# Performance work log

Hardware: AMD Instinct MI355X
Metric: run time of the kernel (lower is better)

Reference implementation:

```python
import jax, jax.numpy as jnp
import numpy as np

MARGIN = 0.25
SCALE = 64.0
OP = 1.0 + MARGIN
ON = -MARGIN
DELTA_P = 1.0 - MARGIN
DELTA_N = MARGIN
NEG_FILL = -1e4  # effectively -inf for these logits (|logit| < ~300)

B, D = 8192, 1024
N_IDS = 512


def setup_inputs() -> dict:
    key = jax.random.key(0)
    k1, k2 = jax.random.split(key)
    inputs = jax.random.normal(k1, (B, D), dtype=jnp.float32)
    targets = jax.random.randint(k2, (B,), 0, N_IDS, dtype=jnp.int64)
    return {"inputs": inputs, "targets": targets}


def reference(inputs, targets):
    # L2-normalize embeddings (torch F.normalize uses eps=1e-12 clamp on norm)
    norm = jnp.maximum(jnp.linalg.norm(inputs, axis=1, keepdims=True), 1e-12)
    x = inputs / norm
    sim = x @ x.T  # [B, B] cosine similarities

    same = targets[:, None] == targets[None, :]
    eye = jnp.eye(targets.shape[0], dtype=bool)
    pos_mask = same & ~eye
    neg_mask = ~same

    sim_sg = jax.lax.stop_gradient(sim)  # .detach() in original
    ap = jnp.maximum(OP - sim_sg, 0.0)
    an = jnp.maximum(sim_sg - ON, 0.0)

    logit_p = -ap * (sim - DELTA_P) * SCALE
    logit_n = an * (sim - DELTA_N) * SCALE

    lse_p = jax.nn.logsumexp(jnp.where(pos_mask, logit_p, NEG_FILL), axis=1)
    lse_n = jax.nn.logsumexp(jnp.where(neg_mask, logit_n, NEG_FILL), axis=1)

    loss_i = jax.nn.softplus(lse_n + lse_p)  # [B]
    valid = pos_mask.any(axis=1) & neg_mask.any(axis=1)

    total = jnp.sum(jnp.where(valid, loss_i, 0.0))
    count = jnp.maximum(jnp.sum(valid), 1)
    return total / count
```

## Files before the change

kernel.cpp:

```cpp
#include <hip/hip_runtime.h>
#include <hip/hip_bf16.h>
#include <math.h>

#define THREADS 256
typedef unsigned short ushortT;
typedef __attribute__((ext_vector_type(8))) short bf16x8;
typedef __attribute__((ext_vector_type(4))) float f32x4;

__device__ __forceinline__ void async16(const ushortT* g, ushortT* l) {
  __builtin_amdgcn_global_load_lds(
      (const __attribute__((address_space(1))) unsigned int*)g,
      (__attribute__((address_space(3))) unsigned int*)l, 16, 0, 0);
}

__device__ __forceinline__ ushortT f2bf(float f) {
  __hip_bfloat16 h = __float2bfloat16(f);
  return *reinterpret_cast<ushortT*>(&h);
}

__global__ __launch_bounds__(THREADS) void k_prep(const float* __restrict__ x,
                                                  ushortT* __restrict__ xn, int D) {
  __shared__ float red[4];
  const int row = blockIdx.x;
  const int tid = threadIdx.x;
  const int gid = row * (D / 4) + tid;
  const float4 v = reinterpret_cast<const float4*>(x)[gid];
  float s = v.x * v.x + v.y * v.y + v.z * v.z + v.w * v.w;
  #pragma unroll
  for (int off = 32; off; off >>= 1) s += __shfl_xor(s, off);
  if ((tid & 63) == 0) red[tid >> 6] = s;
  __syncthreads();
  const float tot = red[0] + red[1] + red[2] + red[3];
  const float rn = 1.0f / fmaxf(sqrtf(tot), 1e-12f);
  ushort4 o;
  o.x = f2bf(v.x * rn); o.y = f2bf(v.y * rn);
  o.z = f2bf(v.z * rn); o.w = f2bf(v.w * rn);
  reinterpret_cast<ushort4*>(xn)[gid] = o;
}

__global__ __launch_bounds__(THREADS, 3) void k_main_mfma(const ushortT* __restrict__ xn,
                                                          const int* __restrict__ tgt,
                                                          float4* __restrict__ partial,
                                                          int D, int nb) {
  __shared__ ushortT Asm[128 * 32];
  __shared__ ushortT Bsm[128 * 32];

  const int tid = threadIdx.x;
  const int lane = tid & 63;
  const int w = tid >> 6;

  const int b = blockIdx.x;
  int bi = (int)((2.f * nb + 1.f -
                  sqrtf((2.f * nb + 1.f) * (2.f * nb + 1.f) - 8.f * (float)b)) * 0.5f);
  while ((bi + 1) * (2 * nb - bi) / 2 <= b) ++bi;
  while (bi * (2 * nb - bi + 1) / 2 > b) --bi;
  const int bj = bi + (b - bi * (2 * nb - bi + 1) / 2);
  const bool isdiag = (bi == bj);

  const int i0 = bi * 128, j0 = bj * 128;
  const int wr = (w >> 1) * 64, wc = (w & 1) * 64;

  const int sr = lane & 15, sc = lane >> 4;
  const ushortT* gA0 = xn + (size_t)(i0 + w * 16 + sr) * D + sc * 8;
  const ushortT* gA1 = gA0 + (size_t)64 * D;
  const ushortT* gB0 = xn + (size_t)(j0 + w * 16 + sr) * D + sc * 8;
  const ushortT* gB1 = gB0 + (size_t)64 * D;
  ushortT* lA0 = &Asm[w * 512];
  ushortT* lA1 = &Asm[(w + 4) * 512];
  ushortT* lB0 = &Bsm[w * 512];
  ushortT* lB1 = &Bsm[(w + 4) * 512];

  const ushortT* Bbase = isdiag ? Asm : Bsm;
  const int aoff = ((w >> 1) * 4) * 512 + lane * 8;
  const int boff = ((w & 1) * 4) * 512 + lane * 8;

  f32x4 acc[4][4];
  #pragma unroll
  for (int mt = 0; mt < 4; ++mt)
    #pragma unroll
    for (int nt = 0; nt < 4; ++nt)
      acc[mt][nt] = (f32x4){0.f, 0.f, 0.f, 0.f};

  const int kiters = D / 32;
  for (int kk = 0; kk < kiters; ++kk) {
    const size_t ko = (size_t)kk * 32;
    async16(gA0 + ko, lA0);
    async16(gA1 + ko, lA1);
    if (!isdiag) {
      async16(gB0 + ko, lB0);
      async16(gB1 + ko, lB1);
    }
    __syncthreads();
    bf16x8 afr[4];
    #pragma unroll
    for (int mt = 0; mt < 4; ++mt)
      afr[mt] = *reinterpret_cast<const bf16x8*>(&Asm[aoff + mt * 512]);
    {
      bf16x8 b0 = *reinterpret_cast<const bf16x8*>(&Bbase[boff]);
      bf16x8 b1 = *reinterpret_cast<const bf16x8*>(&Bbase[boff + 512]);
      #pragma unroll
      for (int mt = 0; mt < 4; ++mt)
        acc[mt][0] = __builtin_amdgcn_mfma_f32_16x16x32_bf16(afr[mt], b0, acc[mt][0], 0, 0, 0);
      #pragma unroll
      for (int mt = 0; mt < 4; ++mt)
        acc[mt][1] = __builtin_amdgcn_mfma_f32_16x16x32_bf16(afr[mt], b1, acc[mt][1], 0, 0, 0);
      b0 = *reinterpret_cast<const bf16x8*>(&Bbase[boff + 2 * 512]);
      b1 = *reinterpret_cast<const bf16x8*>(&Bbase[boff + 3 * 512]);
      #pragma unroll
      for (int mt = 0; mt < 4; ++mt)
        acc[mt][2] = __builtin_amdgcn_mfma_f32_16x16x32_bf16(afr[mt], b0, acc[mt][2], 0, 0, 0);
      #pragma unroll
      for (int mt = 0; mt < 4; ++mt)
        acc[mt][3] = __builtin_amdgcn_mfma_f32_16x16x32_bf16(afr[mt], b1, acc[mt][3], 0, 0, 0);
    }
    __syncthreads();
  }

  const int q = lane >> 4, c = lane & 15;
  int tj[4];
  #pragma unroll
  for (int nt = 0; nt < 4; ++nt) tj[nt] = tgt[j0 + wc + nt * 16 + c];
  int tir[16];
  #pragma unroll
  for (int mt = 0; mt < 4; ++mt) {
    const int4 t4 = *reinterpret_cast<const int4*>(tgt + i0 + wr + mt * 16 + q * 4);
    tir[mt * 4 + 0] = t4.x; tir[mt * 4 + 1] = t4.y;
    tir[mt * 4 + 2] = t4.z; tir[mt * 4 + 3] = t4.w;
  }

  #pragma unroll
  for (int mt = 0; mt < 4; ++mt) {
    #pragma unroll
    for (int reg = 0; reg < 4; ++reg) {
      const int i = i0 + wr + mt * 16 + q * 4 + reg;
      const int ti = tir[mt * 4 + reg];
      float m = -1e30f, sn = 0.f;
      float sel[4];
      #pragma unroll
      for (int nt = 0; nt < 4; ++nt) {
        const float s = acc[mt][nt][reg];
        const int j = j0 + wc + nt * 16 + c;
        const bool same = (tj[nt] == ti);
        const bool vpos = same && (j != i);
        const float lp = (fminf(s, 1.25f) - 1.25f) * fmaf(s, 64.f, -48.f);
        const float sv = vpos ? lp : -2e30f;
        sel[nt] = sv;
        m = fmaxf(m, sv);
        const float ln = (fmaxf(s, -0.25f) + 0.25f) * fmaf(s, 64.f, -16.f);
        const float en = __expf(ln);
        sn += same ? 0.f : en;
      }
      #pragma unroll
      for (int off = 1; off < 16; off <<= 1) m = fmaxf(m, __shfl_xor(m, off));
      float sp = 0.f;
      #pragma unroll
      for (int nt = 0; nt < 4; ++nt) sp += __expf(sel[nt] - m);
      #pragma unroll
      for (int off = 1; off < 16; off <<= 1) {
        sp += __shfl_xor(sp, off);
        sn += __shfl_xor(sn, off);
      }
      if (c == 0) {
        float4 o; o.x = m; o.y = sp; o.z = 0.f; o.w = sn;
        partial[((size_t)i * nb + bj) * 2 + (w & 1)] = o;
      }
    }
  }

  if (!isdiag) {
    #pragma unroll
    for (int nt = 0; nt < 4; ++nt) {
      const int jt = tj[nt];
      const int jrow = j0 + wc + nt * 16 + c;
      float m = -1e30f, sn = 0.f;
      #pragma unroll
      for (int mt = 0; mt < 4; ++mt) {
        #pragma unroll
        for (int reg = 0; reg < 4; ++reg) {
          const float s = acc[mt][nt][reg];
          const bool same = (tir[mt * 4 + reg] == jt);
          const float lp = (fminf(s, 1.25f) - 1.25f) * fmaf(s, 64.f, -48.f);
          m = fmaxf(m, same ? lp : -2e30f);
          const float ln = (fmaxf(s, -0.25f) + 0.25f) * fmaf(s, 64.f, -16.f);
          const float en = __expf(ln);
          sn += same ? 0.f : en;
        }
      }
      m = fmaxf(m, __shfl_xor(m, 16));
      m = fmaxf(m, __shfl_xor(m, 32));
      float sp = 0.f;
      #pragma unroll
      for (int mt = 0; mt < 4; ++mt) {
        #pragma unroll
        for (int reg = 0; reg < 4; ++reg) {
          const float s = acc[mt][nt][reg];
          const bool same = (tir[mt * 4 + reg] == jt);
          const float lp = (fminf(s, 1.25f) - 1.25f) * fmaf(s, 64.f, -48.f);
          sp += __expf((same ? lp : -2e30f) - m);
        }
      }
      sp += __shfl_xor(sp, 16); sp += __shfl_xor(sp, 32);
      sn += __shfl_xor(sn, 16); sn += __shfl_xor(sn, 32);
      if (lane < 16) {
        float4 o; o.x = m; o.y = sp; o.z = 0.f; o.w = sn;
        partial[((size_t)jrow * nb + bi) * 2 + (w >> 1)] = o;
      }
    }
  }
}

__global__ __launch_bounds__(THREADS) void k_reduce(const float4* __restrict__ partial,
                                                    float* __restrict__ row_loss) {
  const int lane = threadIdx.x & 63;
  const int row = blockIdx.x * 4 + (threadIdx.x >> 6);
  const float4 a = partial[(size_t)row * 128 + lane];
  const float4 b = partial[(size_t)row * 128 + 64 + lane];
  float mp = fmaxf(a.x, b.x);
  float sp = a.y * __expf(a.x - mp) + b.y * __expf(b.x - mp);
  float sn = a.w + b.w;
  #pragma unroll
  for (int off = 1; off < 64; off <<= 1) {
    const float m2 = __shfl_xor(mp, off), s2 = __shfl_xor(sp, off);
    const float nm = fmaxf(mp, m2);
    sp = sp * __expf(mp - nm) + s2 * __expf(m2 - nm);
    mp = nm;
    sn += __shfl_xor(sn, off);
  }
  if (lane == 0) {
    float loss = -1.0f;
    if (sp > 0.f && sn > 0.f) {
      const float z = mp + logf(sp) + logf(sn);
      loss = (z > 0.f) ? (z + log1pf(__expf(-z))) : log1pf(__expf(z));
    }
    row_loss[row] = loss;
  }
}

__global__ __launch_bounds__(THREADS) void k_final(const float* __restrict__ row_loss,
                                                   float* __restrict__ out, int B) {
  __shared__ float ssum[4];
  __shared__ float scnt[4];
  const int tid = threadIdx.x;
  float sum = 0.f, cnt = 0.f;
  for (int i = tid; i < B; i += THREADS) {
    const float l = row_loss[i];
    if (l >= 0.f) { sum += l; cnt += 1.f; }
  }
  #pragma unroll
  for (int off = 32; off; off >>= 1) {
    sum += __shfl_xor(sum, off);
    cnt += __shfl_xor(cnt, off);
  }
  if ((tid & 63) == 0) { ssum[tid >> 6] = sum; scnt[tid >> 6] = cnt; }
  __syncthreads();
  if (tid == 0) {
    float ts = 0.f, tc = 0.f;
    #pragma unroll
    for (int w = 0; w < 4; ++w) { ts += ssum[w]; tc += scnt[w]; }
    out[0] = ts / fmaxf(tc, 1.f);
  }
}

extern "C" void kernel_launch(void* const* d_in, const int* in_sizes, int n_in,
                              void* d_out, int out_size, void* d_ws, size_t ws_size,
                              hipStream_t stream) {
  const float* x = (const float*)d_in[0];
  const int* tgt = (const int*)d_in[1];
  float* out = (float*)d_out;
  const int B = in_sizes[1];
  const int D = in_sizes[0] / B;
  const int nb = B / 128;

  ushortT* xn = (ushortT*)d_ws;
  float4* partial = (float4*)((char*)d_ws + (size_t)B * D * 2);
  float* row_loss = (float*)((char*)d_ws + (size_t)B * D * 2 + (size_t)B * 2 * nb * 16);

  k_prep<<<B, THREADS, 0, stream>>>(x, xn, D);
  k_main_mfma<<<nb * (nb + 1) / 2, THREADS, 0, stream>>>(xn, tgt, partial, D, nb);
  k_reduce<<<B / 4, THREADS, 0, stream>>>(partial, row_loss);
  k_final<<<1, THREADS, 0, stream>>>(row_loss, out, B);
}
```

Before: 251.9 us.

## Split 128x128 tile across eight waves with shared-memory merge of row partials

Raises the main MFMA kernel from 4 to 8 waves per block. Each wave now computes a 64x32 sub-tile instead of 64x64 and issues a single async load per operand per k-step. Row-direction partial LSE values from wave pairs are merged in shared memory before being written, so the partial buffer layout stays the same. This aims for more waves per CU to hide latency and to spread the epilogue exp work, at the cost of fewer MFMAs per LDS fragment load and an extra barrier.

```diff
diff --git a/kernel.cpp b/kernel.cpp
--- a/kernel.cpp
+++ b/kernel.cpp
@@ -3,6 +3,7 @@
 #include <math.h>
 
 #define THREADS 256
+#define MTHREADS 512
 typedef unsigned short ushortT;
 typedef __attribute__((ext_vector_type(8))) short bf16x8;
 typedef __attribute__((ext_vector_type(4))) float f32x4;
@@ -38,12 +39,13 @@
   reinterpret_cast<ushort4*>(xn)[gid] = o;
 }
 
-__global__ __launch_bounds__(THREADS, 3) void k_main_mfma(const ushortT* __restrict__ xn,
-                                                          const int* __restrict__ tgt,
-                                                          float4* __restrict__ partial,
-                                                          int D, int nb) {
+__global__ __launch_bounds__(MTHREADS, 4) void k_main_mfma(const ushortT* __restrict__ xn,
+                                                           const int* __restrict__ tgt,
+                                                           float4* __restrict__ partial,
+                                                           int D, int nb) {
   __shared__ ushortT Asm[128 * 32];
   __shared__ ushortT Bsm[128 * 32];
+  __shared__ float4 mrg[8][64];
 
   const int tid = threadIdx.x;
   const int lane = tid & 63;
@@ -58,68 +60,52 @@
   const bool isdiag = (bi == bj);
 
   const int i0 = bi * 128, j0 = bj * 128;
-  const int wr = (w >> 1) * 64, wc = (w & 1) * 64;
+  const int wr = (w >> 2) * 64;
+  const int wc = (w & 3) * 32;
 
   const int sr = lane & 15, sc = lane >> 4;
-  const ushortT* gA0 = xn + (size_t)(i0 + w * 16 + sr) * D + sc * 8;
-  const ushortT* gA1 = gA0 + (size_t)64 * D;
-  const ushortT* gB0 = xn + (size_t)(j0 + w * 16 + sr) * D + sc * 8;
-  const ushortT* gB1 = gB0 + (size_t)64 * D;
-  ushortT* lA0 = &Asm[w * 512];
-  ushortT* lA1 = &Asm[(w + 4) * 512];
-  ushortT* lB0 = &Bsm[w * 512];
-  ushortT* lB1 = &Bsm[(w + 4) * 512];
+  const ushortT* gA = xn + (size_t)(i0 + w * 16 + sr) * D + sc * 8;
+  const ushortT* gB = xn + (size_t)(j0 + w * 16 + sr) * D + sc * 8;
+  ushortT* lA = &Asm[w * 512];
+  ushortT* lB = &Bsm[w * 512];
 
   const ushortT* Bbase = isdiag ? Asm : Bsm;
-  const int aoff = ((w >> 1) * 4) * 512 + lane * 8;
-  const int boff = ((w & 1) * 4) * 512 + lane * 8;
-
-  f32x4 acc[4][4];
+  const int aoff = ((w >> 2) * 4) * 512 + lane * 8;
+  const int boff = ((w & 3) * 2) * 512 + lane * 8;
+
+  f32x4 acc[4][2];
   #pragma unroll
   for (int mt = 0; mt < 4; ++mt)
     #pragma unroll
-    for (int nt = 0; nt < 4; ++nt)
+    for (int nt = 0; nt < 2; ++nt)
       acc[mt][nt] = (f32x4){0.f, 0.f, 0.f, 0.f};
 
   const int kiters = D / 32;
   for (int kk = 0; kk < kiters; ++kk) {
     const size_t ko = (size_t)kk * 32;
-    async16(gA0 + ko, lA0);
-    async16(gA1 + ko, lA1);
-    if (!isdiag) {
-      async16(gB0 + ko, lB0);
-      async16(gB1 + ko, lB1);
-    }
+    async16(gA + ko, lA);
+    if (!isdiag) async16(gB + ko, lB);
     __syncthreads();
     bf16x8 afr[4];
     #pragma unroll
     for (int mt = 0; mt < 4; ++mt)
       afr[mt] = *reinterpret_cast<const bf16x8*>(&Asm[aoff + mt * 512]);
-    {
-      bf16x8 b0 = *reinterpret_cast<const bf16x8*>(&Bbase[boff]);
-      bf16x8 b1 = *reinterpret_cast<const bf16x8*>(&Bbase[boff + 512]);
-      #pragma unroll
-      for (int mt = 0; mt < 4; ++mt)
-        acc[mt][0] = __builtin_amdgcn_mfma_f32_16x16x32_bf16(afr[mt], b0, acc[mt][0], 0, 0, 0);
-      #pragma unroll
-      for (int mt = 0; mt < 4; ++mt)
-        acc[mt][1] = __builtin_amdgcn_mfma_f32_16x16x32_bf16(afr[mt], b1, acc[mt][1], 0, 0, 0);
-      b0 = *reinterpret_cast<const bf16x8*>(&Bbase[boff + 2 * 512]);
-      b1 = *reinterpret_cast<const bf16x8*>(&Bbase[boff + 3 * 512]);
-      #pragma unroll
-      for (int mt = 0; mt < 4; ++mt)
-        acc[mt][2] = __builtin_amdgcn_mfma_f32_16x16x32_bf16(afr[mt], b0, acc[mt][2], 0, 0, 0);
-      #pragma unroll
-      for (int mt = 0; mt < 4; ++mt)
-        acc[mt][3] = __builtin_amdgcn_mfma_f32_16x16x32_bf16(afr[mt], b1, acc[mt][3], 0, 0, 0);
-    }
+    bf16x8 bfr[2];
+    #pragma unroll
+    for (int nt = 0; nt < 2; ++nt)
+      bfr[nt] = *reinterpret_cast<const bf16x8*>(&Bbase[boff + nt * 512]);
+    #pragma unroll
+    for (int mt = 0; mt < 4; ++mt)
+      #pragma unroll
+      for (int nt = 0; nt < 2; ++nt)
+        acc[mt][nt] = __builtin_amdgcn_mfma_f32_16x16x32_bf16(afr[mt], bfr[nt], acc[mt][nt], 0, 0, 0);
     __syncthreads();
   }
 
   const int q = lane >> 4, c = lane & 15;
-  int tj[4];
-  #pragma unroll
-  for (int nt = 0; nt < 4; ++nt) tj[nt] = tgt[j0 + wc + nt * 16 + c];
+  int tj[2];
+  #pragma unroll
+  for (int nt = 0; nt < 2; ++nt) tj[nt] = tgt[j0 + wc + nt * 16 + c];
   int tir[16];
   #pragma unroll
   for (int mt = 0; mt < 4; ++mt) {
@@ -135,9 +121,9 @@
       const int i = i0 + wr + mt * 16 + q * 4 + reg;
       const int ti = tir[mt * 4 + reg];
       float m = -1e30f, sn = 0.f;
-      float sel[4];
-      #pragma unroll
-      for (int nt = 0; nt < 4; ++nt) {
+      float sel[2];
+      #pragma unroll
+      for (int nt = 0; nt < 2; ++nt) {
         const float s = acc[mt][nt][reg];
         const int j = j0 + wc + nt * 16 + c;
         const bool same = (tj[nt] == ti);
@@ -154,7 +140,7 @@
       for (int off = 1; off < 16; off <<= 1) m = fmaxf(m, __shfl_xor(m, off));
       float sp = 0.f;
       #pragma unroll
-      for (int nt = 0; nt < 4; ++nt) sp += __expf(sel[nt] - m);
+      for (int nt = 0; nt < 2; ++nt) sp += __expf(sel[nt] - m);
       #pragma unroll
       for (int off = 1; off < 16; off <<= 1) {
         sp += __shfl_xor(sp, off);
@@ -162,14 +148,24 @@
       }
       if (c == 0) {
         float4 o; o.x = m; o.y = sp; o.z = 0.f; o.w = sn;
-        partial[((size_t)i * nb + bj) * 2 + (w & 1)] = o;
+        mrg[w][mt * 16 + q * 4 + reg] = o;
       }
     }
   }
+  __syncthreads();
+  if (!(w & 1)) {
+    const float4 a = mrg[w][lane];
+    const float4 b2 = mrg[w + 1][lane];
+    const float m = fmaxf(a.x, b2.x);
+    const float sp = a.y * __expf(a.x - m) + b2.y * __expf(b2.x - m);
+    const float sn = a.w + b2.w;
+    float4 o; o.x = m; o.y = sp; o.z = 0.f; o.w = sn;
+    partial[((size_t)(i0 + wr + lane) * nb + bj) * 2 + ((w & 3) >> 1)] = o;
+  }
 
   if (!isdiag) {
     #pragma unroll
-    for (int nt = 0; nt < 4; ++nt) {
+    for (int nt = 0; nt < 2; ++nt) {
       const int jt = tj[nt];
       const int jrow = j0 + wc + nt * 16 + c;
       float m = -1e30f, sn = 0.f;
@@ -203,7 +199,7 @@
       sn += __shfl_xor(sn, 16); sn += __shfl_xor(sn, 32);
       if (lane < 16) {
         float4 o; o.x = m; o.y = sp; o.z = 0.f; o.w = sn;
-        partial[((size_t)jrow * nb + bi) * 2 + (w >> 1)] = o;
+        partial[((size_t)jrow * nb + bi) * 2 + (w >> 2)] = o;
       }
     }
   }
@@ -276,7 +272,7 @@
   float* row_loss = (float*)((char*)d_ws + (size_t)B * D * 2 + (size_t)B * 2 * nb * 16);
 
   k_prep<<<B, THREADS, 0, stream>>>(x, xn, D);
-  k_main_mfma<<<nb * (nb + 1) / 2, THREADS, 0, stream>>>(xn, tgt, partial, D, nb);
+  k_main_mfma<<<nb * (nb + 1) / 2, MTHREADS, 0, stream>>>(xn, tgt, partial, D, nb);
   k_reduce<<<B / 4, THREADS, 0, stream>>>(partial, row_loss);
   k_final<<<1, THREADS, 0, stream>>>(row_loss, out, B);
 }
```

Result: slower. 276.6 us (+9.8%).
